# Optimization experiments

Measured on AMD Instinct MI355X. Metric: run time of the kernel, lower is better.

The kernel has to match this reference:

```python
import jax, jax.numpy as jnp
import numpy as np
import math

N_EMBD = 768
N_HEAD = 12
B, T = 4, 1024


def setup_inputs() -> dict:
    key = jax.random.key(0)
    ks = jax.random.split(key, 12)
    s = 0.02
    d = N_EMBD
    inp = {
        'x': jax.random.normal(ks[0], (B, T, d), dtype=jnp.float32),
        'refractory_state': jax.random.uniform(ks[1], (B, T), dtype=jnp.float32),
        'ln1_w': jnp.ones((d,), jnp.float32),
        'ln1_b': jnp.zeros((d,), jnp.float32),
        'c_attn_w': jax.random.normal(ks[2], (d, 3 * d), dtype=jnp.float32) * s,
        'c_attn_b': jnp.zeros((3 * d,), jnp.float32),
        'c_proj_w': jax.random.normal(ks[3], (d, d), dtype=jnp.float32) * s,
        'c_proj_b': jnp.zeros((d,), jnp.float32),
        'threshold': jnp.full((N_HEAD,), 0.01, jnp.float32),
        'leak': jnp.full((N_HEAD,), 2.0, jnp.float32),
        'steepness': jnp.full((N_HEAD,), 2.0, jnp.float32),
        'refractory_strength': jnp.full((N_HEAD,), -2.0, jnp.float32),
        'cross_layer_weight': jnp.full((N_HEAD,), -2.0, jnp.float32),
        'ln2_w': jnp.ones((d,), jnp.float32),
        'ln2_b': jnp.zeros((d,), jnp.float32),
        'fc_w': jax.random.normal(ks[4], (d, 4 * d), dtype=jnp.float32) * s,
        'fc_b': jnp.zeros((4 * d,), jnp.float32),
        'proj_w': jax.random.normal(ks[5], (4 * d, d), dtype=jnp.float32) * s,
        'proj_b': jnp.zeros((d,), jnp.float32),
    }
    return inp


def _layer_norm(x, w, b, eps=1e-5):
    m = jnp.mean(x, axis=-1, keepdims=True)
    v = jnp.var(x, axis=-1, keepdims=True)
    return (x - m) * jax.lax.rsqrt(v + eps) * w + b


def _per_head(p):
    # [H] -> [1, H, 1, 1]
    return p.reshape(1, -1, 1, 1)


def ember_block(x, refractory_state, ln1_w, ln1_b, c_attn_w, c_attn_b,
                c_proj_w, c_proj_b, threshold, leak, steepness,
                refractory_strength, cross_layer_weight,
                ln2_w, ln2_b, fc_w, fc_b, proj_w, proj_b):
    Bx, Tx, C = x.shape
    hd = C // N_HEAD

    h = _layer_norm(x, ln1_w, ln1_b)
    qkv = h @ c_attn_w + c_attn_b
    q, k, v = jnp.split(qkv, 3, axis=-1)
    # [B, T, C] -> [B, H, T, hd]
    q = q.reshape(Bx, Tx, N_HEAD, hd).transpose(0, 2, 1, 3)
    k = k.reshape(Bx, Tx, N_HEAD, hd).transpose(0, 2, 1, 3)
    v = v.reshape(Bx, Tx, N_HEAD, hd).transpose(0, 2, 1, 3)

    att = jnp.einsum('bhqd,bhkd->bhqk', q, k) * (1.0 / math.sqrt(hd))
    causal = jnp.tril(jnp.ones((Tx, Tx), dtype=bool))
    att = jnp.where(causal, att, -jnp.inf)
    att_probs = jax.nn.softmax(att, axis=-1)

    # per-head LIF modulation with refractory dynamics
    thr = jnp.abs(_per_head(threshold)) * 0.1
    lk = jax.nn.sigmoid(_per_head(leak))
    stp = jax.nn.softplus(_per_head(steepness))

    column_load = att_probs.mean(axis=-2, keepdims=True)  # [B,H,1,T]
    ref_strength = jax.nn.softplus(_per_head(refractory_strength))
    eff_thr = thr + ref_strength * column_load
    cross_w = jax.nn.sigmoid(_per_head(cross_layer_weight))
    prev_load = refractory_state[:, None, None, :]  # [B,1,1,T]
    eff_thr = eff_thr + cross_w * prev_load

    fire_mask = jax.nn.sigmoid(stp * (att_probs - eff_thr))
    lif_weights = fire_mask + lk * (1.0 - fire_mask)
    modulated = att_probs * lif_weights
    modulated = modulated / (modulated.sum(axis=-1, keepdims=True) + 1e-8)
    new_refractory = modulated.mean(axis=1).mean(axis=-2)  # [B,T]

    y = jnp.einsum('bhqk,bhkd->bhqd', modulated, v)
    y = y.transpose(0, 2, 1, 3).reshape(Bx, Tx, C)
    y = y @ c_proj_w + c_proj_b
    x = x + y

    # MLP
    h2 = _layer_norm(x, ln2_w, ln2_b)
    h2 = jax.nn.gelu(h2 @ fc_w + fc_b, approximate=False)
    h2 = h2 @ proj_w + proj_b
    x = x + h2
    return x, new_refractory


def reference(x, refractory_state, ln1_w, ln1_b, c_attn_w, c_attn_b,
              c_proj_w, c_proj_b, threshold, leak, steepness,
              refractory_strength, cross_layer_weight,
              ln2_w, ln2_b, fc_w, fc_b, proj_w, proj_b):
    return ember_block(x, refractory_state, ln1_w, ln1_b, c_attn_w, c_attn_b,
                       c_proj_w, c_proj_b, threshold, leak, steepness,
                       refractory_strength, cross_layer_weight,
                       ln2_w, ln2_b, fc_w, fc_b, proj_w, proj_b)
```

## Files before the change

### kernel.cpp

```cpp
#include <hip/hip_runtime.h>
#include <hip/hip_bf16.h>
#include <math.h>

typedef unsigned short ushort;
typedef __attribute__((ext_vector_type(8))) unsigned short ushort8;
typedef __attribute__((ext_vector_type(8))) short s16x8;
typedef __attribute__((ext_vector_type(4))) float f32x4;

constexpr int NE = 768;
constexpr int NH = 12;
constexpr int HD = 64;
constexpr int Bc = 4;
constexpr int Tc = 1024;
constexpr int BT = Bc * Tc;

__device__ __forceinline__ ushort f2bf(float f) {
    __hip_bfloat16 h = __float2bfloat16(f);
    return *reinterpret_cast<ushort*>(&h);
}
__device__ __forceinline__ float bf2f(ushort u) {
    return __uint_as_float(((unsigned)u) << 16);
}
__device__ __forceinline__ float softplus_f(float x) {
    return (x > 20.f) ? x : log1pf(__expf(x));
}
__device__ __forceinline__ float rcp_f(float x) {
#if __has_builtin(__builtin_amdgcn_rcpf)
    return __builtin_amdgcn_rcpf(x);
#else
    return 1.f / x;
#endif
}
__device__ __forceinline__ void gload16(const void* g, void* l) {
    __builtin_amdgcn_global_load_lds((const __attribute__((address_space(1))) void*)g,
                                     (__attribute__((address_space(3))) void*)l, 16, 0, 0);
}

__global__ __launch_bounds__(256) void ln_kernel(const float* __restrict__ x,
                                                 const float* __restrict__ w,
                                                 const float* __restrict__ b,
                                                 ushort* __restrict__ out) {
    int row = blockIdx.x;
    const float* xr = x + (size_t)row * NE;
    int t = threadIdx.x;
    float v0 = xr[t], v1 = xr[t + 256], v2 = xr[t + 512];
    float s = v0 + v1 + v2;
    float s2 = v0 * v0 + v1 * v1 + v2 * v2;
#pragma unroll
    for (int o = 32; o > 0; o >>= 1) {
        s += __shfl_xor(s, o);
        s2 += __shfl_xor(s2, o);
    }
    __shared__ float ws[4], ws2[4];
    int wv = t >> 6;
    if ((t & 63) == 0) { ws[wv] = s; ws2[wv] = s2; }
    __syncthreads();
    float sum = ws[0] + ws[1] + ws[2] + ws[3];
    float sq = ws2[0] + ws2[1] + ws2[2] + ws2[3];
    float mean = sum * (1.0f / NE);
    float var = sq * (1.0f / NE) - mean * mean;
    float rs = rsqrtf(var + 1e-5f);
    ushort* orow = out + (size_t)row * NE;
    orow[t]       = f2bf((v0 - mean) * rs * w[t]       + b[t]);
    orow[t + 256] = f2bf((v1 - mean) * rs * w[t + 256] + b[t + 256]);
    orow[t + 512] = f2bf((v2 - mean) * rs * w[t + 512] + b[t + 512]);
}

__device__ __forceinline__ void wconv_tile(const float* __restrict__ W,
                                           ushort* __restrict__ Wt,
                                           int K, int N, int bx, int by, int tid) {
    __shared__ float t[32][33];
    int n0 = bx * 32, k0 = by * 32;
    int c = tid & 31, r4 = tid >> 5;
#pragma unroll
    for (int i = 0; i < 4; ++i) {
        int r = r4 + i * 8;
        t[r][c] = W[(size_t)(k0 + r) * N + n0 + c];
    }
    __syncthreads();
#pragma unroll
    for (int i = 0; i < 4; ++i) {
        int r = r4 + i * 8;
        Wt[(size_t)(n0 + r) * K + k0 + c] = f2bf(t[c][r]);
    }
}

__global__ __launch_bounds__(256) void wconvert_all(
    const float* __restrict__ Wa, ushort* __restrict__ Ta,
    const float* __restrict__ Wc, ushort* __restrict__ Tcp,
    const float* __restrict__ Wf, ushort* __restrict__ Tf,
    const float* __restrict__ Wp, ushort* __restrict__ Tp,
    float* __restrict__ colsum, float* __restrict__ refr_out) {
    int blk = blockIdx.x, tid = threadIdx.x;
    if (blk >= 6912) {
        int i = (blk - 6912) * 256 + tid;
        float4 z = make_float4(0.f, 0.f, 0.f, 0.f);
        if (i < 12288) ((float4*)colsum)[i] = z;
        else ((float4*)refr_out)[i - 12288] = z;
        return;
    }
    if (blk < 1728) {
        wconv_tile(Wa, Ta, 768, 2304, blk % 72, blk / 72, tid);
    } else if (blk < 2304) {
        int i = blk - 1728;
        wconv_tile(Wc, Tcp, 768, 768, i % 24, i / 24, tid);
    } else if (blk < 4608) {
        int i = blk - 2304;
        wconv_tile(Wf, Tf, 768, 3072, i % 96, i / 96, tid);
    } else {
        int i = blk - 4608;
        wconv_tile(Wp, Tp, 3072, 768, i % 24, i / 24, tid);
    }
}

template <int BM, int BN, int OUT_MODE, int ACT, bool RES>
__global__ __launch_bounds__(256) void mfma_gemm(
    const ushort* __restrict__ A, const ushort* __restrict__ Bt,
    const float* __restrict__ bias, const float* __restrict__ residual,
    float* __restrict__ Cf, ushort* __restrict__ Cb,
    ushort* __restrict__ Qo, ushort* __restrict__ Ko, ushort* __restrict__ Vo,
    int M, int N, int K, int NBX) {
    constexpr int NF = (BM == 128) ? 4 : 2;
    constexpr int MF = (BM == 64 && BN == 64) ? 2 : 4;
    constexpr int WN = BN / (NF * 16);
    constexpr int APASS = BM / 32, BPASS = BN / 32;
    constexpr bool DBUF = (BM == 64 && BN == 64);
    constexpr int NBUF = DBUF ? 2 : 1;
    __shared__ __align__(16) ushort As[NBUF * BM * 64];
    __shared__ __align__(16) ushort Bs[NBUF * BN * 64];
    int tid = threadIdx.x;
    int lane = tid & 63;
    int nb = gridDim.x;
    int lin = blockIdx.x;
    int nl = (lin & 7) * (nb >> 3) + (lin >> 3);
    int bx = nl % NBX, by = nl / NBX;
    int m0 = by * BM, n0 = bx * BN;
    int wave = tid >> 6;
    int wr = wave / WN, wc = wave % WN;
    f32x4 acc[MF][NF] = {};
    int srow = tid >> 3;
    int scol = (tid & 7) ^ (srow & 7);
    const ushort* ga = A + (size_t)(m0 + srow) * K + scol * 8;
    const ushort* gb = Bt + (size_t)(n0 + srow) * K + scol * 8;
    char* lA = (char*)As + tid * 16;
    char* lB = (char*)Bs + tid * 16;
    int fr = lane & 15, g = lane >> 4;
    unsigned swz = (unsigned)((fr & 7) << 4);
    const char* abase = (const char*)As + (wr * (MF * 16) + fr) * 128;
    const char* bbase = (const char*)Bs + (wc * (NF * 16) + fr) * 128;

    if constexpr (DBUF) {
        constexpr int ABYTES = BM * 64 * 2, BBYTES = BN * 64 * 2;
        int nk = K >> 6;
#pragma unroll
        for (int p = 0; p < APASS; ++p) gload16(ga + (size_t)(p * 32) * K, lA + p * 4096);
#pragma unroll
        for (int p = 0; p < BPASS; ++p) gload16(gb + (size_t)(p * 32) * K, lB + p * 4096);
        for (int k = 0; k < nk; ++k) {
            int cur = k & 1;
            if (k + 1 < nk) {
                int nxt = cur ^ 1;
                int k0 = (k + 1) << 6;
#pragma unroll
                for (int p = 0; p < APASS; ++p)
                    gload16(ga + (size_t)(p * 32) * K + k0, lA + nxt * ABYTES + p * 4096);
#pragma unroll
                for (int p = 0; p < BPASS; ++p)
                    gload16(gb + (size_t)(p * 32) * K + k0, lB + nxt * BBYTES + p * 4096);
                asm volatile("s_waitcnt vmcnt(4)" ::: "memory");
            } else {
                asm volatile("s_waitcnt vmcnt(0)" ::: "memory");
            }
            __builtin_amdgcn_s_barrier();
#pragma unroll
            for (int ks = 0; ks < 2; ++ks) {
                unsigned o = ((unsigned)(g * 16 + ks * 64)) ^ swz;
                s16x8 af[MF], bf[NF];
#pragma unroll
                for (int i = 0; i < MF; ++i)
                    af[i] = *(const s16x8*)(abase + cur * ABYTES + i * 2048 + o);
#pragma unroll
                for (int i = 0; i < NF; ++i)
                    bf[i] = *(const s16x8*)(bbase + cur * BBYTES + i * 2048 + o);
#pragma unroll
                for (int mi = 0; mi < MF; ++mi)
#pragma unroll
                    for (int ni = 0; ni < NF; ++ni)
                        acc[mi][ni] = __builtin_amdgcn_mfma_f32_16x16x32_bf16(af[mi], bf[ni], acc[mi][ni], 0, 0, 0);
            }
            asm volatile("s_waitcnt lgkmcnt(0)" ::: "memory");
            __builtin_amdgcn_s_barrier();
        }
    } else {
        for (int k0 = 0; k0 < K; k0 += 64) {
#pragma unroll
            for (int p = 0; p < APASS; ++p)
                gload16(ga + (size_t)(p * 32) * K + k0, lA + p * 4096);
#pragma unroll
            for (int p = 0; p < BPASS; ++p)
                gload16(gb + (size_t)(p * 32) * K + k0, lB + p * 4096);
            __syncthreads();
#pragma unroll
            for (int ks = 0; ks < 2; ++ks) {
                unsigned o = ((unsigned)(g * 16 + ks * 64)) ^ swz;
                s16x8 af[MF], bf[NF];
#pragma unroll
                for (int i = 0; i < MF; ++i) af[i] = *(const s16x8*)(abase + i * 2048 + o);
#pragma unroll
                for (int i = 0; i < NF; ++i) bf[i] = *(const s16x8*)(bbase + i * 2048 + o);
#pragma unroll
                for (int mi = 0; mi < MF; ++mi)
#pragma unroll
                    for (int ni = 0; ni < NF; ++ni)
                        acc[mi][ni] = __builtin_amdgcn_mfma_f32_16x16x32_bf16(af[mi], bf[ni], acc[mi][ni], 0, 0, 0);
            }
            __syncthreads();
        }
    }
#pragma unroll
    for (int mi = 0; mi < MF; ++mi) {
#pragma unroll
        for (int ni = 0; ni < NF; ++ni) {
#pragma unroll
            for (int j = 0; j < 4; ++j) {
                int row = m0 + wr * (MF * 16) + mi * 16 + g * 4 + j;
                int col = n0 + wc * (NF * 16) + ni * 16 + fr;
                float v = acc[mi][ni][j] + bias[col];
                if (ACT == 1) v = 0.5f * v * (1.0f + erff(v * 0.70710678118654752f));
                if (RES) v += residual[(size_t)row * N + col];
                if (OUT_MODE == 0) {
                    Cf[(size_t)row * N + col] = v;
                } else if (OUT_MODE == 1) {
                    Cb[(size_t)row * N + col] = f2bf(v);
                } else {
                    int which = col >= 1536 ? 2 : (col >= 768 ? 1 : 0);
                    int rem = col - which * 768;
                    int hh = rem >> 6, d = rem & 63;
                    int b_ = row >> 10, t_ = row & 1023;
                    if (which == 2)
                        Vo[((size_t)(b_ * NH + hh) * HD + d) * Tc + t_] = f2bf(v);
                    else {
                        ushort* dst = which == 0 ? Qo : Ko;
                        dst[((size_t)(b_ * NH + hh) * Tc + t_) * HD + d] = f2bf(v);
                    }
                }
            }
        }
    }
}


__global__ __launch_bounds__(128) void attn_P(
    const ushort* __restrict__ Qp, const ushort* __restrict__ Kp,
    ushort* __restrict__ Pbuf, float* __restrict__ denom, float* __restrict__ colsum) {
    int beta = blockIdx.x;
    int tq = 63 - beta / 48;
    int bh = beta % 48;
    int tid = threadIdx.x;
    int kh = tid >> 6, lane = tid & 63, qlane = lane & 15, g = lane >> 4;
    __shared__ ushort plds[2][16][48];
    __shared__ float cs[1056];
    __shared__ float dden[2][16];
    int nst = (tq + 2) >> 1;
    int smid = (nst + 1) >> 1;
    int slo = kh ? smid : 0, shi = kh ? nst : smid;
    int kmaxc = (tq + 1) * 16;
    for (int i = tid; i < 1056; i += 128) cs[i] = 0.f;
    const ushort* Qb = Qp + (size_t)bh * Tc * HD;
    const ushort* Kb = Kp + (size_t)bh * Tc * HD;
    const ushort* qr = Qb + (size_t)(tq * 16 + qlane) * HD + g * 8;
    s16x8 qf0 = *(const s16x8*)qr;
    s16x8 qf1 = *(const s16x8*)(qr + 32);
    ushort* panel = Pbuf + ((size_t)bh * 1056 + (unsigned)(((tq + 1) * (tq + 1)) >> 2)) * 512;
    int q = tq * 16 + qlane;
    s16x8 preg[16];
    float dpart = 0.f;
#pragma unroll
    for (int ss = 0; ss < 16; ++ss) {
        int s = slo + ss;
        if (s < shi) {
            int kt0 = 2 * s, kt1 = 2 * s + 1;
            {
                const ushort* kr = Kb + (size_t)(kt0 * 16 + qlane) * HD + g * 8;
                s16x8 kf0 = *(const s16x8*)kr;
                s16x8 kf1 = *(const s16x8*)(kr + 32);
                f32x4 z = {0.f, 0.f, 0.f, 0.f};
                z = __builtin_amdgcn_mfma_f32_16x16x32_bf16(kf0, qf0, z, 0, 0, 0);
                z = __builtin_amdgcn_mfma_f32_16x16x32_bf16(kf1, qf1, z, 0, 0, 0);
#pragma unroll
                for (int j = 0; j < 4; ++j) {
                    int key = kt0 * 16 + g * 4 + j;
                    float p = (key <= q) ? __expf(z[j] * 0.125f - 8.f) : 0.f;
                    dpart += p;
                    plds[kh][qlane][g * 4 + j] = f2bf(p);
                }
            }
            if (kt1 <= tq) {
                const ushort* kr = Kb + (size_t)(kt1 * 16 + qlane) * HD + g * 8;
                s16x8 kf0 = *(const s16x8*)kr;
                s16x8 kf1 = *(const s16x8*)(kr + 32);
                f32x4 z = {0.f, 0.f, 0.f, 0.f};
                z = __builtin_amdgcn_mfma_f32_16x16x32_bf16(kf0, qf0, z, 0, 0, 0);
                z = __builtin_amdgcn_mfma_f32_16x16x32_bf16(kf1, qf1, z, 0, 0, 0);
#pragma unroll
                for (int j = 0; j < 4; ++j) {
                    int key = kt1 * 16 + g * 4 + j;
                    float p = (key <= q) ? __expf(z[j] * 0.125f - 8.f) : 0.f;
                    dpart += p;
                    plds[kh][qlane][16 + g * 4 + j] = f2bf(p);
                }
            } else {
#pragma unroll
                for (int j = 0; j < 4; ++j) plds[kh][qlane][16 + g * 4 + j] = 0;
            }
            s16x8 pa = *(const s16x8*)&plds[kh][qlane][g * 8];
            preg[ss] = pa;
            *(s16x8*)(panel + (size_t)s * 512 + lane * 8) = pa;
        }
    }
    dpart += __shfl_xor(dpart, 16);
    dpart += __shfl_xor(dpart, 32);
    if (lane < 16) dden[kh][lane] = dpart;
    __syncthreads();
    float dsum = dden[0][qlane] + dden[1][qlane];
    if (tid < 16) denom[(size_t)bh * Tc + tq * 16 + tid] = dden[0][tid] + dden[1][tid];
    float dinvq = rcp_f(dsum);
#pragma unroll
    for (int ss = 0; ss < 16; ++ss) {
        int s = slo + ss;
        if (s < shi) {
            s16x8 v8 = preg[ss];
            int k0 = s * 32 + g * 8;
#pragma unroll
            for (int j = 0; j < 8; ++j) {
                float r = bf2f((ushort)v8[j]) * dinvq;
                r += __shfl_xor(r, 1);
                r += __shfl_xor(r, 2);
                r += __shfl_xor(r, 4);
                r += __shfl_xor(r, 8);
                if (qlane == 0) cs[k0 + j] += r;
            }
        }
    }
    __syncthreads();
    for (int i = tid; i < kmaxc; i += 128)
        atomicAdd(&colsum[(size_t)bh * Tc + i], cs[i]);
}

__global__ __launch_bounds__(128) void attn_CD(
    const ushort* __restrict__ Pbuf, const ushort* __restrict__ Vt,
    const float* __restrict__ denom, const float* __restrict__ colsum,
    const float* __restrict__ refr_in,
    const float* __restrict__ threshold, const float* __restrict__ leak,
    const float* __restrict__ steepness, const float* __restrict__ refr_strength,
    const float* __restrict__ cross_w,
    ushort* __restrict__ ybuf, float* __restrict__ refr_out) {
    int beta = blockIdx.x;
    int tq = 63 - beta / 48;
    int bh = beta % 48;
    int b = bh / NH, h = bh - b * NH;
    int tid = threadIdx.x;
    int kh = tid >> 6, lane = tid & 63, qlane = lane & 15, g = lane >> 4;
    __shared__ float eff[1056];
    __shared__ float cs[1056];
    __shared__ float msum[2][16];
    __shared__ float minvL[16];
    __shared__ float ymrg[16][68];
    int nst = (tq + 2) >> 1;
    int smid = (nst + 1) >> 1;
    int slo = kh ? smid : 0, shi = kh ? nst : smid;
    int kmaxc = (tq + 1) * 16;
    float thr = fabsf(threshold[h]) * 0.1f;
    float lk = 1.f / (1.f + __expf(-leak[h]));
    float lk1m = 1.f - lk;
    float stp = softplus_f(steepness[h]);
    float rfs = softplus_f(refr_strength[h]);
    float crw = 1.f / (1.f + __expf(-cross_w[h]));
    for (int i = tid; i < 1056; i += 128) {
        eff[i] = (i < kmaxc)
                     ? thr + rfs * (colsum[(size_t)bh * Tc + i] * (1.f / 1024.f))
                           + crw * refr_in[(size_t)b * Tc + i]
                     : 0.f;
        cs[i] = 0.f;
    }
    float dinvq = rcp_f(denom[(size_t)bh * Tc + tq * 16 + qlane]);
    __syncthreads();
    const ushort* panel =
        Pbuf + ((size_t)bh * 1056 + (unsigned)(((tq + 1) * (tq + 1)) >> 2)) * 512;
    s16x8 ptreg[16];
    float msp = 0.f;
#pragma unroll
    for (int ss = 0; ss < 16; ++ss) {
        int s = slo + ss;
        if (s < shi) {
            s16x8 v8 = *(const s16x8*)(panel + (size_t)s * 512 + lane * 8);
            int k0 = s * 32 + g * 8;
            s16x8 pw;
#pragma unroll
            for (int j = 0; j < 8; ++j) {
                float p = bf2f((ushort)v8[j]) * dinvq;
                float fire = rcp_f(1.f + __expf(-stp * (p - eff[k0 + j])));
                float pt = p * (lk + lk1m * fire);
                msp += pt;
                pw[j] = (short)f2bf(pt);
            }
            ptreg[ss] = pw;
        }
    }
    msp += __shfl_xor(msp, 16);
    msp += __shfl_xor(msp, 32);
    if (lane < 16) msum[kh][lane] = msp;
    __syncthreads();
    if (tid < 16) minvL[tid] = rcp_f(msum[0][tid] + msum[1][tid] + 1e-8f);
    __syncthreads();
    float minvq = minvL[qlane];
    const ushort* Vh = Vt + (size_t)bh * HD * Tc;
    f32x4 accY[4] = {};
#pragma unroll
    for (int ss = 0; ss < 16; ++ss) {
        int s = slo + ss;
        if (s < shi) {
            s16x8 pa = ptreg[ss];
            int k0 = s * 32 + g * 8;
#pragma unroll
            for (int j = 0; j < 8; ++j) {
                float r = bf2f((ushort)pa[j]) * minvq;
                r += __shfl_xor(r, 1);
                r += __shfl_xor(r, 2);
                r += __shfl_xor(r, 4);
                r += __shfl_xor(r, 8);
                if (qlane == 0) cs[k0 + j] += r;
            }
#pragma unroll
            for (int dt = 0; dt < 4; ++dt) {
                const ushort* vp = Vh + (size_t)(dt * 16 + qlane) * Tc + s * 32 + g * 8;
                s16x8 vf = *(const s16x8*)vp;
                accY[dt] = __builtin_amdgcn_mfma_f32_16x16x32_bf16(pa, vf, accY[dt], 0, 0, 0);
            }
        }
    }
    if (kh == 1) {
#pragma unroll
        for (int dt = 0; dt < 4; ++dt)
#pragma unroll
            for (int j = 0; j < 4; ++j)
                ymrg[g * 4 + j][dt * 16 + qlane] = accY[dt][j];
    }
    __syncthreads();
    if (kh == 0) {
#pragma unroll
        for (int dt = 0; dt < 4; ++dt)
#pragma unroll
            for (int j = 0; j < 4; ++j) {
                float y = (accY[dt][j] + ymrg[g * 4 + j][dt * 16 + qlane]) * minvL[g * 4 + j];
                ybuf[(size_t)(b * Tc + tq * 16 + g * 4 + j) * NE + h * 64 + dt * 16 + qlane] =
                    f2bf(y);
            }
    }
    for (int i = tid; i < kmaxc; i += 128)
        atomicAdd(&refr_out[(size_t)b * Tc + i], cs[i] * (1.f / (NH * Tc)));
}

extern "C" void kernel_launch(void* const* d_in, const int* in_sizes, int n_in,
                              void* d_out, int out_size, void* d_ws, size_t ws_size,
                              hipStream_t stream) {
    const float* x        = (const float*)d_in[0];
    const float* refr     = (const float*)d_in[1];
    const float* ln1_w    = (const float*)d_in[2];
    const float* ln1_b    = (const float*)d_in[3];
    const float* c_attn_w = (const float*)d_in[4];
    const float* c_attn_b = (const float*)d_in[5];
    const float* c_proj_w = (const float*)d_in[6];
    const float* c_proj_b = (const float*)d_in[7];
    const float* threshold = (const float*)d_in[8];
    const float* leak      = (const float*)d_in[9];
    const float* steepness = (const float*)d_in[10];
    const float* refractory_strength = (const float*)d_in[11];
    const float* cross_layer_weight  = (const float*)d_in[12];
    const float* ln2_w    = (const float*)d_in[13];
    const float* ln2_b    = (const float*)d_in[14];
    const float* fc_w     = (const float*)d_in[15];
    const float* fc_b     = (const float*)d_in[16];
    const float* proj_w   = (const float*)d_in[17];
    const float* proj_b   = (const float*)d_in[18];

    char* ws = (char*)d_ws;
    ushort* hbuf   = (ushort*)(ws + 0);
    ushort* qb     = (ushort*)(ws + 6291456);
    ushort* kb     = (ushort*)(ws + 12582912);
    ushort* vtg    = (ushort*)(ws + 18874368);
    ushort* ybuf   = (ushort*)(ws + 25165824);
    ushort* fc_act = (ushort*)(ws + 6291456);
    float*  denomb = (float*)(ws + 31457280);
    float*  colsum = (float*)(ws + 31653888);
    ushort* wt_attn  = (ushort*)(ws + 31850496);
    ushort* wt_cproj = (ushort*)(ws + 35389440);
    ushort* wt_fc    = (ushort*)(ws + 36569088);
    ushort* wt_proj  = (ushort*)(ws + 41287680);
    ushort* Pbuf     = (ushort*)(ws + 46006272);

    float* xout = (float*)d_out;
    float* refr_out = xout + (size_t)BT * NE;

    wconvert_all<<<6964, 256, 0, stream>>>(c_attn_w, wt_attn, c_proj_w, wt_cproj,
                                           fc_w, wt_fc, proj_w, wt_proj,
                                           colsum, refr_out);

    ln_kernel<<<BT, 256, 0, stream>>>(x, ln1_w, ln1_b, hbuf);

    mfma_gemm<64, 128, 2, 0, false><<<1152, 256, 0, stream>>>(
        hbuf, wt_attn, c_attn_b, nullptr, nullptr, nullptr, qb, kb, vtg,
        BT, 3 * NE, NE, 18);

    attn_P<<<48 * 64, 128, 0, stream>>>(qb, kb, Pbuf, denomb, colsum);
    attn_CD<<<48 * 64, 128, 0, stream>>>(
        Pbuf, vtg, denomb, colsum, refr, threshold, leak, steepness,
        refractory_strength, cross_layer_weight, ybuf, refr_out);

    mfma_gemm<64, 64, 0, 0, true><<<768, 256, 0, stream>>>(
        ybuf, wt_cproj, c_proj_b, x, xout, nullptr, nullptr, nullptr, nullptr,
        BT, NE, NE, 12);

    ln_kernel<<<BT, 256, 0, stream>>>(xout, ln2_w, ln2_b, hbuf);

    mfma_gemm<128, 128, 1, 1, false><<<768, 256, 0, stream>>>(
        hbuf, wt_fc, fc_b, nullptr, nullptr, fc_act, nullptr, nullptr, nullptr,
        BT, 4 * NE, NE, 24);

    mfma_gemm<64, 64, 0, 0, true><<<768, 256, 0, stream>>>(
        fc_act, wt_proj, proj_b, xout, xout, nullptr, nullptr, nullptr, nullptr,
        BT, NE, 4 * NE, 12);
}
```

Baseline: 241.3 us.

## Split-K the MLP down-projection with atomics and fold LN1 into weight conversion

The final 3072-deep projection GEMM is split into two K halves across twice as many blocks. Each half atomically adds into the output, which already holds the residual, and only the first split adds the bias. Separately, the first LayerNorm is merged into the weight-conversion launch as extra blocks, removing one kernel launch. Split-K raises parallelism for the long-K GEMM but adds fp32 atomic traffic and makes the summation order nondeterministic.

Measured after the change: 256.0 us. 6.1% more time.

```diff
diff --git a/kernel.cpp b/kernel.cpp
--- a/kernel.cpp
+++ b/kernel.cpp
@@ -36,13 +36,11 @@
                                      (__attribute__((address_space(3))) void*)l, 16, 0, 0);
 }
 
-__global__ __launch_bounds__(256) void ln_kernel(const float* __restrict__ x,
-                                                 const float* __restrict__ w,
-                                                 const float* __restrict__ b,
-                                                 ushort* __restrict__ out) {
-    int row = blockIdx.x;
+__device__ __forceinline__ void ln_row(const float* __restrict__ x,
+                                       const float* __restrict__ w,
+                                       const float* __restrict__ b,
+                                       ushort* __restrict__ out, int row, int t) {
     const float* xr = x + (size_t)row * NE;
-    int t = threadIdx.x;
     float v0 = xr[t], v1 = xr[t + 256], v2 = xr[t + 512];
     float s = v0 + v1 + v2;
     float s2 = v0 * v0 + v1 * v1 + v2 * v2;
@@ -51,12 +49,12 @@
         s += __shfl_xor(s, o);
         s2 += __shfl_xor(s2, o);
     }
-    __shared__ float ws[4], ws2[4];
+    __shared__ float lws[4], lws2[4];
     int wv = t >> 6;
-    if ((t & 63) == 0) { ws[wv] = s; ws2[wv] = s2; }
-    __syncthreads();
-    float sum = ws[0] + ws[1] + ws[2] + ws[3];
-    float sq = ws2[0] + ws2[1] + ws2[2] + ws2[3];
+    if ((t & 63) == 0) { lws[wv] = s; lws2[wv] = s2; }
+    __syncthreads();
+    float sum = lws[0] + lws[1] + lws[2] + lws[3];
+    float sq = lws2[0] + lws2[1] + lws2[2] + lws2[3];
     float mean = sum * (1.0f / NE);
     float var = sq * (1.0f / NE) - mean * mean;
     float rs = rsqrtf(var + 1e-5f);
@@ -66,6 +64,13 @@
     orow[t + 512] = f2bf((v2 - mean) * rs * w[t + 512] + b[t + 512]);
 }
 
+__global__ __launch_bounds__(256) void ln_kernel(const float* __restrict__ x,
+                                                 const float* __restrict__ w,
+                                                 const float* __restrict__ b,
+                                                 ushort* __restrict__ out) {
+    ln_row(x, w, b, out, blockIdx.x, threadIdx.x);
+}
+
 __device__ __forceinline__ void wconv_tile(const float* __restrict__ W,
                                            ushort* __restrict__ Wt,
                                            int K, int N, int bx, int by, int tid) {
@@ -90,8 +95,14 @@
     const float* __restrict__ Wc, ushort* __restrict__ Tcp,
     const float* __restrict__ Wf, ushort* __restrict__ Tf,
     const float* __restrict__ Wp, ushort* __restrict__ Tp,
-    float* __restrict__ colsum, float* __restrict__ refr_out) {
+    float* __restrict__ colsum, float* __restrict__ refr_out,
+    const float* __restrict__ x, const float* __restrict__ ln1_w,
+    const float* __restrict__ ln1_b, ushort* __restrict__ hbuf) {
     int blk = blockIdx.x, tid = threadIdx.x;
+    if (blk >= 6964) {
+        ln_row(x, ln1_w, ln1_b, hbuf, blk - 6964, tid);
+        return;
+    }
     if (blk >= 6912) {
         int i = (blk - 6912) * 256 + tid;
         float4 z = make_float4(0.f, 0.f, 0.f, 0.f);
@@ -119,7 +130,7 @@
     const float* __restrict__ bias, const float* __restrict__ residual,
     float* __restrict__ Cf, ushort* __restrict__ Cb,
     ushort* __restrict__ Qo, ushort* __restrict__ Ko, ushort* __restrict__ Vo,
-    int M, int N, int K, int NBX) {
+    int M, int N, int K, int NBX, int KLD, int NSPLIT) {
     constexpr int NF = (BM == 128) ? 4 : 2;
     constexpr int MF = (BM == 64 && BN == 64) ? 2 : 4;
     constexpr int WN = BN / (NF * 16);
@@ -133,15 +144,19 @@
     int nb = gridDim.x;
     int lin = blockIdx.x;
     int nl = (lin & 7) * (nb >> 3) + (lin >> 3);
-    int bx = nl % NBX, by = nl / NBX;
+    int nper = nb / NSPLIT;
+    int sp = nl / nper;
+    int rem2 = nl - sp * nper;
+    int bx = rem2 % NBX, by = rem2 / NBX;
     int m0 = by * BM, n0 = bx * BN;
+    int kbase = sp * K;
     int wave = tid >> 6;
     int wr = wave / WN, wc = wave % WN;
     f32x4 acc[MF][NF] = {};
     int srow = tid >> 3;
     int scol = (tid & 7) ^ (srow & 7);
-    const ushort* ga = A + (size_t)(m0 + srow) * K + scol * 8;
-    const ushort* gb = Bt + (size_t)(n0 + srow) * K + scol * 8;
+    const ushort* ga = A + (size_t)(m0 + srow) * KLD + kbase + scol * 8;
+    const ushort* gb = Bt + (size_t)(n0 + srow) * KLD + kbase + scol * 8;
     char* lA = (char*)As + tid * 16;
     char* lB = (char*)Bs + tid * 16;
     int fr = lane & 15, g = lane >> 4;
@@ -153,9 +168,9 @@
         constexpr int ABYTES = BM * 64 * 2, BBYTES = BN * 64 * 2;
         int nk = K >> 6;
 #pragma unroll
-        for (int p = 0; p < APASS; ++p) gload16(ga + (size_t)(p * 32) * K, lA + p * 4096);
-#pragma unroll
-        for (int p = 0; p < BPASS; ++p) gload16(gb + (size_t)(p * 32) * K, lB + p * 4096);
+        for (int p = 0; p < APASS; ++p) gload16(ga + (size_t)(p * 32) * KLD, lA + p * 4096);
+#pragma unroll
+        for (int p = 0; p < BPASS; ++p) gload16(gb + (size_t)(p * 32) * KLD, lB + p * 4096);
         for (int k = 0; k < nk; ++k) {
             int cur = k & 1;
             if (k + 1 < nk) {
@@ -163,10 +178,10 @@
                 int k0 = (k + 1) << 6;
 #pragma unroll
                 for (int p = 0; p < APASS; ++p)
-                    gload16(ga + (size_t)(p * 32) * K + k0, lA + nxt * ABYTES + p * 4096);
+                    gload16(ga + (size_t)(p * 32) * KLD + k0, lA + nxt * ABYTES + p * 4096);
 #pragma unroll
                 for (int p = 0; p < BPASS; ++p)
-                    gload16(gb + (size_t)(p * 32) * K + k0, lB + nxt * BBYTES + p * 4096);
+                    gload16(gb + (size_t)(p * 32) * KLD + k0, lB + nxt * BBYTES + p * 4096);
                 asm volatile("s_waitcnt vmcnt(4)" ::: "memory");
             } else {
                 asm volatile("s_waitcnt vmcnt(0)" ::: "memory");
@@ -195,10 +210,10 @@
         for (int k0 = 0; k0 < K; k0 += 64) {
 #pragma unroll
             for (int p = 0; p < APASS; ++p)
-                gload16(ga + (size_t)(p * 32) * K + k0, lA + p * 4096);
+                gload16(ga + (size_t)(p * 32) * KLD + k0, lA + p * 4096);
 #pragma unroll
             for (int p = 0; p < BPASS; ++p)
-                gload16(gb + (size_t)(p * 32) * K + k0, lB + p * 4096);
+                gload16(gb + (size_t)(p * 32) * KLD + k0, lB + p * 4096);
             __syncthreads();
 #pragma unroll
             for (int ks = 0; ks < 2; ++ks) {
@@ -225,13 +240,17 @@
             for (int j = 0; j < 4; ++j) {
                 int row = m0 + wr * (MF * 16) + mi * 16 + g * 4 + j;
                 int col = n0 + wc * (NF * 16) + ni * 16 + fr;
-                float v = acc[mi][ni][j] + bias[col];
+                float v = acc[mi][ni][j];
+                if (OUT_MODE != 3) v += bias[col];
+                else if (sp == 0) v += bias[col];
                 if (ACT == 1) v = 0.5f * v * (1.0f + erff(v * 0.70710678118654752f));
                 if (RES) v += residual[(size_t)row * N + col];
                 if (OUT_MODE == 0) {
                     Cf[(size_t)row * N + col] = v;
                 } else if (OUT_MODE == 1) {
                     Cb[(size_t)row * N + col] = f2bf(v);
+                } else if (OUT_MODE == 3) {
+                    atomicAdd(&Cf[(size_t)row * N + col], v);
                 } else {
                     int which = col >= 1536 ? 2 : (col >= 768 ? 1 : 0);
                     int rem = col - which * 768;
@@ -502,15 +521,13 @@
     float* xout = (float*)d_out;
     float* refr_out = xout + (size_t)BT * NE;
 
-    wconvert_all<<<6964, 256, 0, stream>>>(c_attn_w, wt_attn, c_proj_w, wt_cproj,
-                                           fc_w, wt_fc, proj_w, wt_proj,
-                                           colsum, refr_out);
-
-    ln_kernel<<<BT, 256, 0, stream>>>(x, ln1_w, ln1_b, hbuf);
+    wconvert_all<<<11060, 256, 0, stream>>>(c_attn_w, wt_attn, c_proj_w, wt_cproj,
+                                            fc_w, wt_fc, proj_w, wt_proj,
+                                            colsum, refr_out, x, ln1_w, ln1_b, hbuf);
 
     mfma_gemm<64, 128, 2, 0, false><<<1152, 256, 0, stream>>>(
         hbuf, wt_attn, c_attn_b, nullptr, nullptr, nullptr, qb, kb, vtg,
-        BT, 3 * NE, NE, 18);
+        BT, 3 * NE, NE, 18, NE, 1);
 
     attn_P<<<48 * 64, 128, 0, stream>>>(qb, kb, Pbuf, denomb, colsum);
     attn_CD<<<48 * 64, 128, 0, stream>>>(
@@ -519,15 +536,15 @@
 
     mfma_gemm<64, 64, 0, 0, true><<<768, 256, 0, stream>>>(
         ybuf, wt_cproj, c_proj_b, x, xout, nullptr, nullptr, nullptr, nullptr,
-        BT, NE, NE, 12);
+        BT, NE, NE, 12, NE, 1);
 
     ln_kernel<<<BT, 256, 0, stream>>>(xout, ln2_w, ln2_b, hbuf);
 
     mfma_gemm<128, 128, 1, 1, false><<<768, 256, 0, stream>>>(
         hbuf, wt_fc, fc_b, nullptr, nullptr, fc_act, nullptr, nullptr, nullptr,
-        BT, 4 * NE, NE, 24);
-
-    mfma_gemm<64, 64, 0, 0, true><<<768, 256, 0, stream>>>(
-        fc_act, wt_proj, proj_b, xout, xout, nullptr, nullptr, nullptr, nullptr,
-        BT, NE, 4 * NE, 12);
-}
+        BT, 4 * NE, NE, 24, NE, 1);
+
+    mfma_gemm<64, 64, 3, 0, false><<<1536, 256, 0, stream>>>(
+        fc_act, wt_proj, proj_b, nullptr, xout, nullptr, nullptr, nullptr, nullptr,
+        BT, NE, 4 * NE / 2, 12, 4 * NE, 2);
+}
```
